# Optimization experiments

Hardware: AMD Instinct MI355X
Metric: run time of the kernel (lower is better)

Reference implementation:

```python
import jax, jax.numpy as jnp
import numpy as np

N_NODES = 50000
N_EDGES = 800000
D_IN = 128
D_HID = 128
N_CLASSES = 40


def setup_inputs() -> dict:
    key = jax.random.key(0)
    ks = jax.random.split(key, 12)
    x = jax.random.normal(ks[0], (N_NODES, D_IN), dtype=jnp.float32)
    edge_index = jax.random.randint(ks[1], (2, N_EDGES), 0, N_NODES, dtype=jnp.int64)
    s1 = 1.0 / np.sqrt(D_IN)
    s2 = 1.0 / np.sqrt(D_HID)
    W1 = jax.random.uniform(ks[2], (D_IN, D_HID), jnp.float32, -s1, s1)
    b1 = jnp.zeros((D_HID,), jnp.float32)
    W2 = jax.random.uniform(ks[3], (D_HID, D_HID), jnp.float32, -s2, s2)
    b2 = jnp.zeros((D_HID,), jnp.float32)
    W3 = jax.random.uniform(ks[4], (D_HID, D_HID), jnp.float32, -s2, s2)
    b3 = jnp.zeros((D_HID,), jnp.float32)
    fcW = jax.random.uniform(ks[5], (D_HID, N_CLASSES), jnp.float32, -s2, s2)
    fcb = jax.random.uniform(ks[6], (N_CLASSES,), jnp.float32, -s2, s2)
    return {"x": x, "edge_index": edge_index, "W1": W1, "b1": b1,
            "W2": W2, "b2": b2, "W3": W3, "b3": b3, "fcW": fcW, "fcb": fcb}


def _gcn_norm(edge_index, n_nodes):
    # add self-loops, compute symmetric normalization deg^-1/2[src]*deg^-1/2[dst]
    loops = jnp.arange(n_nodes, dtype=edge_index.dtype)
    src = jnp.concatenate([edge_index[0], loops])
    dst = jnp.concatenate([edge_index[1], loops])
    deg = jax.ops.segment_sum(jnp.ones_like(dst, dtype=jnp.float32), dst,
                              num_segments=n_nodes)
    dinv = jax.lax.rsqrt(deg)  # deg >= 1 thanks to self-loops
    norm = dinv[src] * dinv[dst]  # [E+N]
    return src, dst, norm


def _gcn_conv(h, W, b, src, dst, norm, n_nodes):
    h = h @ W                               # [N, D]
    msg = h[src] * norm[:, None]            # [E+N, D] gather + scale
    out = jax.ops.segment_sum(msg, dst, num_segments=n_nodes)  # scatter-add
    return out + b


def reference(x, edge_index, W1, b1, W2, b2, W3, b3, fcW, fcb):
    n = x.shape[0]
    src, dst, norm = _gcn_norm(edge_index, n)
    h = jax.nn.relu(_gcn_conv(x, W1, b1, src, dst, norm, n))
    h = jax.nn.relu(_gcn_conv(h, W2, b2, src, dst, norm, n))
    h = jax.nn.relu(_gcn_conv(h, W3, b3, src, dst, norm, n))
    out = h @ fcW + fcb
    return (h, out)
```

## Files before the change

### kernel.cpp

```cpp
#include <hip/hip_runtime.h>
#include <hip/hip_fp16.h>

#define NN 50000
#define NE 800000
#define D  128
#define NC 40
#define NBLK ((NN + 255) / 256)
#define NXCD 8
#define DRANGE ((NN + NXCD - 1) / NXCD)
#define EPB 2048
#define NCH ((NE + EPB - 1) / EPB)
#define CAP 64

typedef short bf16x8 __attribute__((ext_vector_type(8)));
typedef float f32x16 __attribute__((ext_vector_type(16)));

__device__ __forceinline__ void load_edge(const void* ei, int e, int is64, int& s, int& d) {
    if (is64) {
        const long long* p = (const long long*)ei;
        s = (int)p[e]; d = (int)p[NE + e];
    } else {
        const int* p = (const int*)ei;
        s = p[e]; d = p[NE + e];
    }
}

__global__ __launch_bounds__(256) void init_cnt_kernel(int* __restrict__ cnt) {
    int i = blockIdx.x * 256 + threadIdx.x;
    if (i < NN) cnt[i] = 0;
}

__global__ void detect_kernel(const int* ei, int* flag) {
    __shared__ int nz;
    if (threadIdx.x == 0) nz = 0;
    __syncthreads();
    int c = 0;
    for (int i = threadIdx.x; i < 2048; i += 256)
        if (ei[2 * i + 1] != 0) c = 1;
    if (c) atomicAdd(&nz, 1);
    __syncthreads();
    if (threadIdx.x == 0) *flag = (nz == 0) ? 1 : 0;
}

__global__ __launch_bounds__(256) void fill_kernel(const void* ei, const int* __restrict__ flag,
                                                   int* cnt, int* __restrict__ srcs) {
    int r = blockIdx.x & (NXCD - 1);
    int chunk = blockIdx.x >> 3;
    int base = chunk * EPB;
    int dlo = r * DRANGE, dhi = dlo + DRANGE;
    int is64 = *flag;
#pragma unroll
    for (int j = 0; j < EPB / 256; ++j) {
        int e = base + threadIdx.x + j * 256;
        if (e >= NE) break;
        int s, d; load_edge(ei, e, is64, s, d);
        if (d < dlo || d >= dhi || (unsigned)d >= NN || (unsigned)s >= NN) continue;
        int slot = atomicAdd(&cnt[d], 1);
        if (slot < CAP) srcs[d * CAP + slot] = s;
    }
}

__global__ __launch_bounds__(256) void sort_kernel(const int* __restrict__ cnt,
                                                   int* __restrict__ srcs) {
    int wid = (blockIdx.x * 256 + threadIdx.x) >> 6;
    int lane = threadIdx.x & 63;
    if (wid >= NN) return;
    int deg = cnt[wid]; if (deg > CAP) deg = CAP;
    if (deg <= 1) return;
    int base = wid * CAP;
    int v = (lane < deg) ? srcs[base + lane] : 0x7fffffff;
#pragma unroll
    for (int k = 2; k <= 64; k <<= 1) {
#pragma unroll
        for (int j = k >> 1; j > 0; j >>= 1) {
            int o = __shfl_xor(v, j);
            bool up = ((lane & k) == 0);
            bool lower = ((lane & j) == 0);
            int mn = min(v, o), mx = max(v, o);
            v = (lower == up) ? mn : mx;
        }
    }
    if (lane < deg) srcs[base + lane] = v;
}

__global__ __launch_bounds__(256) void dinv_kernel(const int* __restrict__ cnt,
                                                   float* __restrict__ dinv) {
    int i = blockIdx.x * 256 + threadIdx.x;
    if (i < NN) dinv[i] = 1.0f / sqrtf((float)cnt[i] + 1.0f);
}

__device__ __forceinline__ ushort f2bf(float x) {
    unsigned u = __float_as_uint(x);
    return (ushort)((u + 0x7fffu + ((u >> 16) & 1u)) >> 16);
}
__device__ __forceinline__ float bf2f(ushort h) {
    return __uint_as_float(((unsigned)h) << 16);
}

__global__ __launch_bounds__(128) void prep_w_kernel(const float* __restrict__ W,
                                                     ushort* __restrict__ img) {
    int c = blockIdx.x;
    int k = threadIdx.x;
    float w = W[(size_t)k * D + c];
    ushort hi = f2bf(w);
    ushort lo = f2bf(w - bf2f(hi));
    int ch = k >> 6, kk = k & 63, g = kk >> 3;
    int idx = c * 64 + ((g ^ (c & 7)) * 8) + (kk & 7);
    img[(size_t)(ch * 2 + 0) * 8192 + idx] = hi;
    img[(size_t)(ch * 2 + 1) * 8192 + idx] = lo;
}

__global__ __launch_bounds__(128) void prep_fcw_kernel(const float* __restrict__ W,
                                                       ushort* __restrict__ img) {
    int c = blockIdx.x;
    int k = threadIdx.x;
    float w = (c < NC) ? W[(size_t)k * NC + c] : 0.0f;
    ushort hi = f2bf(w);
    ushort lo = f2bf(w - bf2f(hi));
    int g = k >> 3;
    int idx = c * 128 + ((g ^ (c & 7)) * 8) + (k & 7);
    img[idx] = hi;
    img[8192 + idx] = lo;
}

__global__ __launch_bounds__(256, 2) void gemm_mfma_kernel(const float* __restrict__ A,
                                                           const ushort* __restrict__ Wimg,
                                                           ushort* __restrict__ T) {
    __shared__ alignas(16) ushort sAh[8192];
    __shared__ alignas(16) ushort sAl[8192];
    __shared__ alignas(16) ushort sWh[8192];
    __shared__ alignas(16) ushort sWl[8192];
    int tid = threadIdx.x;
    int wave = tid >> 6, lane = tid & 63;
    int wr = wave >> 1, wc = wave & 1;
    int m0 = blockIdx.x * 128;
    f32x16 acc[2][2];
#pragma unroll
    for (int i = 0; i < 2; ++i)
#pragma unroll
        for (int j = 0; j < 2; ++j)
#pragma unroll
            for (int q = 0; q < 16; ++q) acc[i][j][q] = 0.0f;

    for (int ch = 0; ch < 2; ++ch) {
        const float4* wh = (const float4*)(Wimg + (size_t)(ch * 2 + 0) * 8192);
        const float4* wl = (const float4*)(Wimg + (size_t)(ch * 2 + 1) * 8192);
#pragma unroll
        for (int i = 0; i < 4; ++i) {
            ((float4*)sWh)[tid + i * 256] = wh[tid + i * 256];
            ((float4*)sWl)[tid + i * 256] = wl[tid + i * 256];
        }
#pragma unroll
        for (int p = 0; p < 8; ++p) {
            int idx = tid + p * 256;
            int r = idx >> 4;
            int kq = idx & 15;
            float4 v = make_float4(0, 0, 0, 0);
            int grow = m0 + r;
            if (grow < NN) v = *(const float4*)(A + (size_t)grow * D + ch * 64 + kq * 4);
            ushort4 h, l;
            h.x = f2bf(v.x); l.x = f2bf(v.x - bf2f(h.x));
            h.y = f2bf(v.y); l.y = f2bf(v.y - bf2f(h.y));
            h.z = f2bf(v.z); l.z = f2bf(v.z - bf2f(h.z));
            h.w = f2bf(v.w); l.w = f2bf(v.w - bf2f(h.w));
            int g = kq >> 1, half = kq & 1;
            int uidx = r * 64 + ((g ^ (r & 7)) * 8) + half * 4;
            *(ushort4*)&sAh[uidx] = h;
            *(ushort4*)&sAl[uidx] = l;
        }
        __syncthreads();

        int rb = wr * 64 + (lane & 31);
        int cb = wc * 64 + (lane & 31);
#pragma unroll
        for (int s = 0; s < 4; ++s) {
            int gg = s * 2 + (lane >> 5);
            int ra0 = rb, ra1 = rb + 32;
            int ca0 = cb, ca1 = cb + 32;
            bf16x8 ah0 = *(const bf16x8*)&sAh[ra0 * 64 + ((gg ^ (ra0 & 7)) * 8)];
            bf16x8 ah1 = *(const bf16x8*)&sAh[ra1 * 64 + ((gg ^ (ra1 & 7)) * 8)];
            bf16x8 al0 = *(const bf16x8*)&sAl[ra0 * 64 + ((gg ^ (ra0 & 7)) * 8)];
            bf16x8 al1 = *(const bf16x8*)&sAl[ra1 * 64 + ((gg ^ (ra1 & 7)) * 8)];
            bf16x8 wh0 = *(const bf16x8*)&sWh[ca0 * 64 + ((gg ^ (ca0 & 7)) * 8)];
            bf16x8 wh1 = *(const bf16x8*)&sWh[ca1 * 64 + ((gg ^ (ca1 & 7)) * 8)];
            bf16x8 wl0 = *(const bf16x8*)&sWl[ca0 * 64 + ((gg ^ (ca0 & 7)) * 8)];
            bf16x8 wl1 = *(const bf16x8*)&sWl[ca1 * 64 + ((gg ^ (ca1 & 7)) * 8)];
            acc[0][0] = __builtin_amdgcn_mfma_f32_32x32x16_bf16(ah0, wh0, acc[0][0], 0, 0, 0);
            acc[0][0] = __builtin_amdgcn_mfma_f32_32x32x16_bf16(ah0, wl0, acc[0][0], 0, 0, 0);
            acc[0][0] = __builtin_amdgcn_mfma_f32_32x32x16_bf16(al0, wh0, acc[0][0], 0, 0, 0);
            acc[0][1] = __builtin_amdgcn_mfma_f32_32x32x16_bf16(ah0, wh1, acc[0][1], 0, 0, 0);
            acc[0][1] = __builtin_amdgcn_mfma_f32_32x32x16_bf16(ah0, wl1, acc[0][1], 0, 0, 0);
            acc[0][1] = __builtin_amdgcn_mfma_f32_32x32x16_bf16(al0, wh1, acc[0][1], 0, 0, 0);
            acc[1][0] = __builtin_amdgcn_mfma_f32_32x32x16_bf16(ah1, wh0, acc[1][0], 0, 0, 0);
            acc[1][0] = __builtin_amdgcn_mfma_f32_32x32x16_bf16(ah1, wl0, acc[1][0], 0, 0, 0);
            acc[1][0] = __builtin_amdgcn_mfma_f32_32x32x16_bf16(al1, wh0, acc[1][0], 0, 0, 0);
            acc[1][1] = __builtin_amdgcn_mfma_f32_32x32x16_bf16(ah1, wh1, acc[1][1], 0, 0, 0);
            acc[1][1] = __builtin_amdgcn_mfma_f32_32x32x16_bf16(ah1, wl1, acc[1][1], 0, 0, 0);
            acc[1][1] = __builtin_amdgcn_mfma_f32_32x32x16_bf16(al1, wh1, acc[1][1], 0, 0, 0);
        }
        __syncthreads();
    }
#pragma unroll
    for (int rt = 0; rt < 2; ++rt)
#pragma unroll
        for (int ct = 0; ct < 2; ++ct) {
            int cg = wc * 64 + ct * 32 + (lane & 31);
#pragma unroll
            for (int reg = 0; reg < 16; ++reg) {
                int row = m0 + wr * 64 + rt * 32 + (reg & 3) + 8 * (reg >> 2) + 4 * (lane >> 5);
                if (row < NN)
                    T[(size_t)row * D + cg] = __half_as_ushort(__float2half(acc[rt][ct][reg]));
            }
        }
}

__global__ __launch_bounds__(256, 2) void fc_mfma_kernel(const float* __restrict__ A,
                                                         const ushort* __restrict__ img,
                                                         const float* __restrict__ b,
                                                         float* __restrict__ O) {
    __shared__ alignas(16) ushort sAh[8192];
    __shared__ alignas(16) ushort sAl[8192];
    __shared__ alignas(16) ushort sWh[8192];
    __shared__ alignas(16) ushort sWl[8192];
    int tid = threadIdx.x;
    int wave = tid >> 6, lane = tid & 63;
    int m0 = blockIdx.x * 128;
#pragma unroll
    for (int i = 0; i < 4; ++i) {
        ((float4*)sWh)[tid + i * 256] = ((const float4*)img)[tid + i * 256];
        ((float4*)sWl)[tid + i * 256] = ((const float4*)(img + 8192))[tid + i * 256];
    }
    f32x16 acc[2];
#pragma unroll
    for (int j = 0; j < 2; ++j)
#pragma unroll
        for (int q = 0; q < 16; ++q) acc[j][q] = 0.0f;

    for (int ch = 0; ch < 2; ++ch) {
#pragma unroll
        for (int p = 0; p < 8; ++p) {
            int idx = tid + p * 256;
            int r = idx >> 4;
            int kq = idx & 15;
            float4 v = make_float4(0, 0, 0, 0);
            int grow = m0 + r;
            if (grow < NN) v = *(const float4*)(A + (size_t)grow * D + ch * 64 + kq * 4);
            ushort4 h, l;
            h.x = f2bf(v.x); l.x = f2bf(v.x - bf2f(h.x));
            h.y = f2bf(v.y); l.y = f2bf(v.y - bf2f(h.y));
            h.z = f2bf(v.z); l.z = f2bf(v.z - bf2f(h.z));
            h.w = f2bf(v.w); l.w = f2bf(v.w - bf2f(h.w));
            int g = kq >> 1, half = kq & 1;
            int uidx = r * 64 + ((g ^ (r & 7)) * 8) + half * 4;
            *(ushort4*)&sAh[uidx] = h;
            *(ushort4*)&sAl[uidx] = l;
        }
        __syncthreads();
        int ra = wave * 32 + (lane & 31);
        int c0 = lane & 31, c1 = 32 + (lane & 31);
#pragma unroll
        for (int s = 0; s < 4; ++s) {
            int gg = s * 2 + (lane >> 5);
            int kg = ch * 8 + gg;
            bf16x8 ah = *(const bf16x8*)&sAh[ra * 64 + ((gg ^ (ra & 7)) * 8)];
            bf16x8 al = *(const bf16x8*)&sAl[ra * 64 + ((gg ^ (ra & 7)) * 8)];
            bf16x8 wh0 = *(const bf16x8*)&sWh[c0 * 128 + ((kg ^ (c0 & 7)) * 8)];
            bf16x8 wl0 = *(const bf16x8*)&sWl[c0 * 128 + ((kg ^ (c0 & 7)) * 8)];
            bf16x8 wh1 = *(const bf16x8*)&sWh[c1 * 128 + ((kg ^ (c1 & 7)) * 8)];
            bf16x8 wl1 = *(const bf16x8*)&sWl[c1 * 128 + ((kg ^ (c1 & 7)) * 8)];
            acc[0] = __builtin_amdgcn_mfma_f32_32x32x16_bf16(ah, wh0, acc[0], 0, 0, 0);
            acc[0] = __builtin_amdgcn_mfma_f32_32x32x16_bf16(ah, wl0, acc[0], 0, 0, 0);
            acc[0] = __builtin_amdgcn_mfma_f32_32x32x16_bf16(al, wh0, acc[0], 0, 0, 0);
            acc[1] = __builtin_amdgcn_mfma_f32_32x32x16_bf16(ah, wh1, acc[1], 0, 0, 0);
            acc[1] = __builtin_amdgcn_mfma_f32_32x32x16_bf16(ah, wl1, acc[1], 0, 0, 0);
            acc[1] = __builtin_amdgcn_mfma_f32_32x32x16_bf16(al, wh1, acc[1], 0, 0, 0);
        }
        __syncthreads();
    }
#pragma unroll
    for (int ct = 0; ct < 2; ++ct) {
        int col = ct * 32 + (lane & 31);
        if (col < NC) {
            float bb = b[col];
#pragma unroll
            for (int reg = 0; reg < 16; ++reg) {
                int row = m0 + wave * 32 + (reg & 3) + 8 * (reg >> 2) + 4 * (lane >> 5);
                if (row < NN) O[(size_t)row * NC + col] = acc[ct][reg] + bb;
            }
        }
    }
}

__device__ __forceinline__ float4 h4load(const ushort* __restrict__ T, int row, int l) {
    uint2 hv = ((const uint2*)(T + (size_t)row * D))[l];
    __half2 h0 = *(__half2*)&hv.x, h1 = *(__half2*)&hv.y;
    float2 f0 = __half22float2(h0), f1 = __half22float2(h1);
    return make_float4(f0.x, f0.y, f1.x, f1.y);
}

__global__ __launch_bounds__(256) void aggregate_kernel(const ushort* __restrict__ T,
                                                        const int* __restrict__ cnt,
                                                        const int* __restrict__ srcs,
                                                        const float* __restrict__ dinv,
                                                        const float* __restrict__ b,
                                                        float* __restrict__ out) {
    int wid = (blockIdx.x * 256 + threadIdx.x) >> 6;
    int lane = threadIdx.x & 63;
    int h = lane >> 5, l = lane & 31;
    if (wid >= NN) return;
    float di = dinv[wid];
    float wself = h ? 0.0f : di * di;
    float4 acc = h4load(T, wid, l);
    acc.x *= wself; acc.y *= wself; acc.z *= wself; acc.w *= wself;
    int beg = wid * CAP;
    int deg = cnt[wid]; if (deg > CAP) deg = CAP;
    int end = beg + deg;
    int e = beg;
    for (; e + 7 < end; e += 8) {
        int s0 = srcs[e + h], s1 = srcs[e + 2 + h];
        int s2 = srcs[e + 4 + h], s3 = srcs[e + 6 + h];
        float w0 = dinv[s0] * di, w1 = dinv[s1] * di;
        float w2 = dinv[s2] * di, w3 = dinv[s3] * di;
        float4 v0 = h4load(T, s0, l);
        float4 v1 = h4load(T, s1, l);
        float4 v2 = h4load(T, s2, l);
        float4 v3 = h4load(T, s3, l);
        acc.x = fmaf(v0.x, w0, acc.x); acc.y = fmaf(v0.y, w0, acc.y);
        acc.z = fmaf(v0.z, w0, acc.z); acc.w = fmaf(v0.w, w0, acc.w);
        acc.x = fmaf(v1.x, w1, acc.x); acc.y = fmaf(v1.y, w1, acc.y);
        acc.z = fmaf(v1.z, w1, acc.z); acc.w = fmaf(v1.w, w1, acc.w);
        acc.x = fmaf(v2.x, w2, acc.x); acc.y = fmaf(v2.y, w2, acc.y);
        acc.z = fmaf(v2.z, w2, acc.z); acc.w = fmaf(v2.w, w2, acc.w);
        acc.x = fmaf(v3.x, w3, acc.x); acc.y = fmaf(v3.y, w3, acc.y);
        acc.z = fmaf(v3.z, w3, acc.z); acc.w = fmaf(v3.w, w3, acc.w);
    }
    for (; e + 1 < end; e += 2) {
        int s0 = srcs[e + h];
        float w0 = dinv[s0] * di;
        float4 v0 = h4load(T, s0, l);
        acc.x = fmaf(v0.x, w0, acc.x); acc.y = fmaf(v0.y, w0, acc.y);
        acc.z = fmaf(v0.z, w0, acc.z); acc.w = fmaf(v0.w, w0, acc.w);
    }
    if (e < end) {
        int ee = (e + h < end) ? e + h : end - 1;
        int s0 = srcs[ee];
        float w0 = (e + h < end) ? dinv[s0] * di : 0.0f;
        float4 v0 = h4load(T, s0, l);
        acc.x = fmaf(v0.x, w0, acc.x); acc.y = fmaf(v0.y, w0, acc.y);
        acc.z = fmaf(v0.z, w0, acc.z); acc.w = fmaf(v0.w, w0, acc.w);
    }
    acc.x += __shfl_xor(acc.x, 32);
    acc.y += __shfl_xor(acc.y, 32);
    acc.z += __shfl_xor(acc.z, 32);
    acc.w += __shfl_xor(acc.w, 32);
    if (h == 0) {
        float4 bb = ((const float4*)b)[l];
        acc.x = fmaxf(acc.x + bb.x, 0.0f);
        acc.y = fmaxf(acc.y + bb.y, 0.0f);
        acc.z = fmaxf(acc.z + bb.z, 0.0f);
        acc.w = fmaxf(acc.w + bb.w, 0.0f);
        ((float4*)(out + (size_t)wid * D))[l] = acc;
    }
}

extern "C" void kernel_launch(void* const* d_in, const int* in_sizes, int n_in,
                              void* d_out, int out_size, void* d_ws, size_t ws_size,
                              hipStream_t stream) {
    const float* x   = (const float*)d_in[0];
    const void*  ei  = d_in[1];
    const float* W1  = (const float*)d_in[2];
    const float* b1  = (const float*)d_in[3];
    const float* W2  = (const float*)d_in[4];
    const float* b2  = (const float*)d_in[5];
    const float* W3  = (const float*)d_in[6];
    const float* b3  = (const float*)d_in[7];
    const float* fcW = (const float*)d_in[8];
    const float* fcb = (const float*)d_in[9];

    float* out_h  = (float*)d_out;
    float* out_fc = out_h + (size_t)NN * D;

    size_t off = 0;
    auto alloc = [&](size_t bytes) {
        void* p = (char*)d_ws + off;
        off += (bytes + 255) & ~(size_t)255;
        return p;
    };
    float*  dinv   = (float*) alloc((size_t)NN * 4);
    int*    cnt    = (int*)   alloc((size_t)NN * 4);
    int*    flag   = (int*)   alloc(256);
    int*    srcs   = (int*)   alloc((size_t)NN * CAP * 4);
    ushort* bufT   = (ushort*)alloc((size_t)NN * D * 2);
    float*  bufH   = (float*) alloc((size_t)NN * D * 4);
    ushort* wimg1  = (ushort*)alloc(32768 * 2);
    ushort* wimg2  = (ushort*)alloc(32768 * 2);
    ushort* wimg3  = (ushort*)alloc(32768 * 2);
    ushort* fcimg  = (ushort*)alloc(16384 * 2);
    (void)ws_size; (void)in_sizes; (void)n_in; (void)out_size;

    init_cnt_kernel<<<NBLK, 256, 0, stream>>>(cnt);
    detect_kernel<<<1, 256, 0, stream>>>((const int*)ei, flag);
    prep_w_kernel<<<128, 128, 0, stream>>>(W1, wimg1);
    prep_w_kernel<<<128, 128, 0, stream>>>(W2, wimg2);
    prep_w_kernel<<<128, 128, 0, stream>>>(W3, wimg3);
    prep_fcw_kernel<<<64, 128, 0, stream>>>(fcW, fcimg);
    fill_kernel<<<NCH * NXCD, 256, 0, stream>>>(ei, flag, cnt, srcs);
    sort_kernel<<<(NN * 64 + 255) / 256, 256, 0, stream>>>(cnt, srcs);
    dinv_kernel<<<NBLK, 256, 0, stream>>>(cnt, dinv);

    auto layer = [&](const float* in, const ushort* wimg, const float* b, float* out) {
        gemm_mfma_kernel<<<(NN + 127) / 128, 256, 0, stream>>>(in, wimg, bufT);
        aggregate_kernel<<<(NN * 64 + 255) / 256, 256, 0, stream>>>(bufT, cnt, srcs, dinv, b, out);
    };

    layer(x,    wimg1, b1, bufH);
    layer(bufH, wimg2, b2, bufH);
    layer(bufH, wimg3, b3, out_h);

    fc_mfma_kernel<<<(NN + 127) / 128, 256, 0, stream>>>(out_h, fcimg, fcb, out_fc);
}
```

Before: 248.5 us.

## Emit pre-split bf16 tile images from aggregation and merge setup kernels

The hidden-layer aggregation now writes its output directly as a swizzled, tiled bf16 hi/lo split image, so the next GEMM can load its A tile straight into shared memory without a float-to-bf16 split pass. The float intermediate buffer is removed. Setup work is also consolidated: count init and int64 detection share one launch, the four weight-prep launches become one, and the dinv computation is folded into the sort kernel. Together these cut launch overhead and per-GEMM conversion work, at the cost of more template and layout complexity.

```diff
diff --git a/kernel.cpp b/kernel.cpp
--- a/kernel.cpp
+++ b/kernel.cpp
@@ -11,6 +11,7 @@
 #define EPB 2048
 #define NCH ((NE + EPB - 1) / EPB)
 #define CAP 64
+#define NTILE ((NN + 127) / 128)
 
 typedef short bf16x8 __attribute__((ext_vector_type(8)));
 typedef float f32x16 __attribute__((ext_vector_type(16)));
@@ -25,21 +26,23 @@
     }
 }
 
-__global__ __launch_bounds__(256) void init_cnt_kernel(int* __restrict__ cnt) {
-    int i = blockIdx.x * 256 + threadIdx.x;
-    if (i < NN) cnt[i] = 0;
-}
-
-__global__ void detect_kernel(const int* ei, int* flag) {
-    __shared__ int nz;
-    if (threadIdx.x == 0) nz = 0;
-    __syncthreads();
-    int c = 0;
-    for (int i = threadIdx.x; i < 2048; i += 256)
-        if (ei[2 * i + 1] != 0) c = 1;
-    if (c) atomicAdd(&nz, 1);
-    __syncthreads();
-    if (threadIdx.x == 0) *flag = (nz == 0) ? 1 : 0;
+__global__ __launch_bounds__(256) void setup_kernel(int* __restrict__ cnt,
+                                                    const int* __restrict__ ei,
+                                                    int* __restrict__ flag) {
+    if (blockIdx.x == NBLK) {
+        __shared__ int nz;
+        if (threadIdx.x == 0) nz = 0;
+        __syncthreads();
+        int c = 0;
+        for (int i = threadIdx.x; i < 2048; i += 256)
+            if (ei[2 * i + 1] != 0) c = 1;
+        if (c) atomicAdd(&nz, 1);
+        __syncthreads();
+        if (threadIdx.x == 0) *flag = (nz == 0) ? 1 : 0;
+    } else {
+        int i = blockIdx.x * 256 + threadIdx.x;
+        if (i < NN) cnt[i] = 0;
+    }
 }
 
 __global__ __launch_bounds__(256) void fill_kernel(const void* ei, const int* __restrict__ flag,
@@ -61,11 +64,14 @@
 }
 
 __global__ __launch_bounds__(256) void sort_kernel(const int* __restrict__ cnt,
-                                                   int* __restrict__ srcs) {
+                                                   int* __restrict__ srcs,
+                                                   float* __restrict__ dinv) {
     int wid = (blockIdx.x * 256 + threadIdx.x) >> 6;
     int lane = threadIdx.x & 63;
     if (wid >= NN) return;
-    int deg = cnt[wid]; if (deg > CAP) deg = CAP;
+    int deg_raw = cnt[wid];
+    if (lane == 0) dinv[wid] = 1.0f / sqrtf((float)deg_raw + 1.0f);
+    int deg = (deg_raw > CAP) ? CAP : deg_raw;
     if (deg <= 1) return;
     int base = wid * CAP;
     int v = (lane < deg) ? srcs[base + lane] : 0x7fffffff;
@@ -83,12 +89,6 @@
     if (lane < deg) srcs[base + lane] = v;
 }
 
-__global__ __launch_bounds__(256) void dinv_kernel(const int* __restrict__ cnt,
-                                                   float* __restrict__ dinv) {
-    int i = blockIdx.x * 256 + threadIdx.x;
-    if (i < NN) dinv[i] = 1.0f / sqrtf((float)cnt[i] + 1.0f);
-}
-
 __device__ __forceinline__ ushort f2bf(float x) {
     unsigned u = __float_as_uint(x);
     return (ushort)((u + 0x7fffu + ((u >> 16) & 1u)) >> 16);
@@ -97,35 +97,43 @@
     return __uint_as_float(((unsigned)h) << 16);
 }
 
-__global__ __launch_bounds__(128) void prep_w_kernel(const float* __restrict__ W,
-                                                     ushort* __restrict__ img) {
-    int c = blockIdx.x;
+__global__ __launch_bounds__(128) void prep_all_kernel(const float* __restrict__ W1,
+                                                       const float* __restrict__ W2,
+                                                       const float* __restrict__ W3,
+                                                       const float* __restrict__ fcW,
+                                                       ushort* __restrict__ i1,
+                                                       ushort* __restrict__ i2,
+                                                       ushort* __restrict__ i3,
+                                                       ushort* __restrict__ ifc) {
+    int b = blockIdx.x;
     int k = threadIdx.x;
-    float w = W[(size_t)k * D + c];
-    ushort hi = f2bf(w);
-    ushort lo = f2bf(w - bf2f(hi));
-    int ch = k >> 6, kk = k & 63, g = kk >> 3;
-    int idx = c * 64 + ((g ^ (c & 7)) * 8) + (kk & 7);
-    img[(size_t)(ch * 2 + 0) * 8192 + idx] = hi;
-    img[(size_t)(ch * 2 + 1) * 8192 + idx] = lo;
-}
-
-__global__ __launch_bounds__(128) void prep_fcw_kernel(const float* __restrict__ W,
-                                                       ushort* __restrict__ img) {
-    int c = blockIdx.x;
-    int k = threadIdx.x;
-    float w = (c < NC) ? W[(size_t)k * NC + c] : 0.0f;
-    ushort hi = f2bf(w);
-    ushort lo = f2bf(w - bf2f(hi));
-    int g = k >> 3;
-    int idx = c * 128 + ((g ^ (c & 7)) * 8) + (k & 7);
-    img[idx] = hi;
-    img[8192 + idx] = lo;
-}
-
-__global__ __launch_bounds__(256, 2) void gemm_mfma_kernel(const float* __restrict__ A,
-                                                           const ushort* __restrict__ Wimg,
-                                                           ushort* __restrict__ T) {
+    if (b < 384) {
+        const float* W = (b < 128) ? W1 : (b < 256) ? W2 : W3;
+        ushort* img = (b < 128) ? i1 : (b < 256) ? i2 : i3;
+        int c = b & 127;
+        float w = W[(size_t)k * D + c];
+        ushort hi = f2bf(w);
+        ushort lo = f2bf(w - bf2f(hi));
+        int ch = k >> 6, kk = k & 63, g = kk >> 3;
+        int idx = c * 64 + ((g ^ (c & 7)) * 8) + (kk & 7);
+        img[(size_t)(ch * 2 + 0) * 8192 + idx] = hi;
+        img[(size_t)(ch * 2 + 1) * 8192 + idx] = lo;
+    } else {
+        int c = b - 384;
+        float w = (c < NC) ? fcW[(size_t)k * NC + c] : 0.0f;
+        ushort hi = f2bf(w);
+        ushort lo = f2bf(w - bf2f(hi));
+        int g = k >> 3;
+        int idx = c * 128 + ((g ^ (c & 7)) * 8) + (k & 7);
+        ifc[idx] = hi;
+        ifc[8192 + idx] = lo;
+    }
+}
+
+
+__global__ __launch_bounds__(256, 2) void gemm_f32_kernel(const float* __restrict__ A,
+                                                          const ushort* __restrict__ Wimg,
+                                                          ushort* __restrict__ T) {
     __shared__ alignas(16) ushort sAh[8192];
     __shared__ alignas(16) ushort sAl[8192];
     __shared__ alignas(16) ushort sWh[8192];
@@ -214,6 +222,84 @@
         }
 }
 
+__global__ __launch_bounds__(256, 2) void gemm_img_kernel(const ushort* __restrict__ Aimg,
+                                                          const ushort* __restrict__ Wimg,
+                                                          ushort* __restrict__ T) {
+    __shared__ alignas(16) ushort sAh[8192];
+    __shared__ alignas(16) ushort sAl[8192];
+    __shared__ alignas(16) ushort sWh[8192];
+    __shared__ alignas(16) ushort sWl[8192];
+    int tid = threadIdx.x;
+    int wave = tid >> 6, lane = tid & 63;
+    int wr = wave >> 1, wc = wave & 1;
+    int m0 = blockIdx.x * 128;
+    const ushort* Atile = Aimg + (size_t)blockIdx.x * 32768;
+    f32x16 acc[2][2];
+#pragma unroll
+    for (int i = 0; i < 2; ++i)
+#pragma unroll
+        for (int j = 0; j < 2; ++j)
+#pragma unroll
+            for (int q = 0; q < 16; ++q) acc[i][j][q] = 0.0f;
+
+    for (int ch = 0; ch < 2; ++ch) {
+        const float4* wh = (const float4*)(Wimg + (size_t)(ch * 2 + 0) * 8192);
+        const float4* wl = (const float4*)(Wimg + (size_t)(ch * 2 + 1) * 8192);
+        const float4* ah = (const float4*)(Atile + (size_t)(ch * 2 + 0) * 8192);
+        const float4* al = (const float4*)(Atile + (size_t)(ch * 2 + 1) * 8192);
+#pragma unroll
+        for (int i = 0; i < 4; ++i) {
+            ((float4*)sWh)[tid + i * 256] = wh[tid + i * 256];
+            ((float4*)sWl)[tid + i * 256] = wl[tid + i * 256];
+            ((float4*)sAh)[tid + i * 256] = ah[tid + i * 256];
+            ((float4*)sAl)[tid + i * 256] = al[tid + i * 256];
+        }
+        __syncthreads();
+
+        int rb = wr * 64 + (lane & 31);
+        int cb = wc * 64 + (lane & 31);
+#pragma unroll
+        for (int s = 0; s < 4; ++s) {
+            int gg = s * 2 + (lane >> 5);
+            int ra0 = rb, ra1 = rb + 32;
+            int ca0 = cb, ca1 = cb + 32;
+            bf16x8 ah0 = *(const bf16x8*)&sAh[ra0 * 64 + ((gg ^ (ra0 & 7)) * 8)];
+            bf16x8 ah1 = *(const bf16x8*)&sAh[ra1 * 64 + ((gg ^ (ra1 & 7)) * 8)];
+            bf16x8 al0 = *(const bf16x8*)&sAl[ra0 * 64 + ((gg ^ (ra0 & 7)) * 8)];
+            bf16x8 al1 = *(const bf16x8*)&sAl[ra1 * 64 + ((gg ^ (ra1 & 7)) * 8)];
+            bf16x8 wh0 = *(const bf16x8*)&sWh[ca0 * 64 + ((gg ^ (ca0 & 7)) * 8)];
+            bf16x8 wh1 = *(const bf16x8*)&sWh[ca1 * 64 + ((gg ^ (ca1 & 7)) * 8)];
+            bf16x8 wl0 = *(const bf16x8*)&sWl[ca0 * 64 + ((gg ^ (ca0 & 7)) * 8)];
+            bf16x8 wl1 = *(const bf16x8*)&sWl[ca1 * 64 + ((gg ^ (ca1 & 7)) * 8)];
+            acc[0][0] = __builtin_amdgcn_mfma_f32_32x32x16_bf16(ah0, wh0, acc[0][0], 0, 0, 0);
+            acc[0][0] = __builtin_amdgcn_mfma_f32_32x32x16_bf16(ah0, wl0, acc[0][0], 0, 0, 0);
+            acc[0][0] = __builtin_amdgcn_mfma_f32_32x32x16_bf16(al0, wh0, acc[0][0], 0, 0, 0);
+            acc[0][1] = __builtin_amdgcn_mfma_f32_32x32x16_bf16(ah0, wh1, acc[0][1], 0, 0, 0);
+            acc[0][1] = __builtin_amdgcn_mfma_f32_32x32x16_bf16(ah0, wl1, acc[0][1], 0, 0, 0);
+            acc[0][1] = __builtin_amdgcn_mfma_f32_32x32x16_bf16(al0, wh1, acc[0][1], 0, 0, 0);
+            acc[1][0] = __builtin_amdgcn_mfma_f32_32x32x16_bf16(ah1, wh0, acc[1][0], 0, 0, 0);
+            acc[1][0] = __builtin_amdgcn_mfma_f32_32x32x16_bf16(ah1, wl0, acc[1][0], 0, 0, 0);
+            acc[1][0] = __builtin_amdgcn_mfma_f32_32x32x16_bf16(al1, wh0, acc[1][0], 0, 0, 0);
+            acc[1][1] = __builtin_amdgcn_mfma_f32_32x32x16_bf16(ah1, wh1, acc[1][1], 0, 0, 0);
+            acc[1][1] = __builtin_amdgcn_mfma_f32_32x32x16_bf16(ah1, wl1, acc[1][1], 0, 0, 0);
+            acc[1][1] = __builtin_amdgcn_mfma_f32_32x32x16_bf16(al1, wh1, acc[1][1], 0, 0, 0);
+        }
+        __syncthreads();
+    }
+#pragma unroll
+    for (int rt = 0; rt < 2; ++rt)
+#pragma unroll
+        for (int ct = 0; ct < 2; ++ct) {
+            int cg = wc * 64 + ct * 32 + (lane & 31);
+#pragma unroll
+            for (int reg = 0; reg < 16; ++reg) {
+                int row = m0 + wr * 64 + rt * 32 + (reg & 3) + 8 * (reg >> 2) + 4 * (lane >> 5);
+                if (row < NN)
+                    T[(size_t)row * D + cg] = __half_as_ushort(__float2half(acc[rt][ct][reg]));
+            }
+        }
+}
+
 __global__ __launch_bounds__(256, 2) void fc_mfma_kernel(const float* __restrict__ A,
                                                          const ushort* __restrict__ img,
                                                          const float* __restrict__ b,
@@ -298,12 +384,14 @@
     return make_float4(f0.x, f0.y, f1.x, f1.y);
 }
 
+template<int IMG>
 __global__ __launch_bounds__(256) void aggregate_kernel(const ushort* __restrict__ T,
                                                         const int* __restrict__ cnt,
                                                         const int* __restrict__ srcs,
                                                         const float* __restrict__ dinv,
                                                         const float* __restrict__ b,
-                                                        float* __restrict__ out) {
+                                                        float* __restrict__ out,
+                                                        ushort* __restrict__ img) {
     int wid = (blockIdx.x * 256 + threadIdx.x) >> 6;
     int lane = threadIdx.x & 63;
     int h = lane >> 5, l = lane & 31;
@@ -359,7 +447,22 @@
         acc.y = fmaxf(acc.y + bb.y, 0.0f);
         acc.z = fmaxf(acc.z + bb.z, 0.0f);
         acc.w = fmaxf(acc.w + bb.w, 0.0f);
-        ((float4*)(out + (size_t)wid * D))[l] = acc;
+        if (IMG) {
+            int tile = wid >> 7, rr = wid & 127;
+            int c0 = 4 * l;
+            int ch = c0 >> 6, kk = c0 & 63, g = kk >> 3;
+            int idx = rr * 64 + ((g ^ (rr & 7)) * 8) + (kk & 7);
+            ushort4 hh, ll;
+            hh.x = f2bf(acc.x); ll.x = f2bf(acc.x - bf2f(hh.x));
+            hh.y = f2bf(acc.y); ll.y = f2bf(acc.y - bf2f(hh.y));
+            hh.z = f2bf(acc.z); ll.z = f2bf(acc.z - bf2f(hh.z));
+            hh.w = f2bf(acc.w); ll.w = f2bf(acc.w - bf2f(hh.w));
+            ushort* base = img + (size_t)tile * 32768;
+            *(ushort4*)(base + (size_t)(ch * 2 + 0) * 8192 + idx) = hh;
+            *(ushort4*)(base + (size_t)(ch * 2 + 1) * 8192 + idx) = ll;
+        } else {
+            ((float4*)(out + (size_t)wid * D))[l] = acc;
+        }
     }
 }
 
@@ -391,31 +494,25 @@
     int*    flag   = (int*)   alloc(256);
     int*    srcs   = (int*)   alloc((size_t)NN * CAP * 4);
     ushort* bufT   = (ushort*)alloc((size_t)NN * D * 2);
-    float*  bufH   = (float*) alloc((size_t)NN * D * 4);
+    ushort* himg   = (ushort*)alloc((size_t)NTILE * 32768 * 2);
     ushort* wimg1  = (ushort*)alloc(32768 * 2);
     ushort* wimg2  = (ushort*)alloc(32768 * 2);
     ushort* wimg3  = (ushort*)alloc(32768 * 2);
     ushort* fcimg  = (ushort*)alloc(16384 * 2);
     (void)ws_size; (void)in_sizes; (void)n_in; (void)out_size;
 
-    init_cnt_kernel<<<NBLK, 256, 0, stream>>>(cnt);
-    detect_kernel<<<1, 256, 0, stream>>>((const int*)ei, flag);
-    prep_w_kernel<<<128, 128, 0, stream>>>(W1, wimg1);
-    prep_w_kernel<<<128, 128, 0, stream>>>(W2, wimg2);
-    prep_w_kernel<<<128, 128, 0, stream>>>(W3, wimg3);
-    prep_fcw_kernel<<<64, 128, 0, stream>>>(fcW, fcimg);
+    setup_kernel<<<NBLK + 1, 256, 0, stream>>>(cnt, (const int*)ei, flag);
+    prep_all_kernel<<<448, 128, 0, stream>>>(W1, W2, W3, fcW, wimg1, wimg2, wimg3, fcimg);
     fill_kernel<<<NCH * NXCD, 256, 0, stream>>>(ei, flag, cnt, srcs);
-    sort_kernel<<<(NN * 64 + 255) / 256, 256, 0, stream>>>(cnt, srcs);
-    dinv_kernel<<<NBLK, 256, 0, stream>>>(cnt, dinv);
-
-    auto layer = [&](const float* in, const ushort* wimg, const float* b, float* out) {
-        gemm_mfma_kernel<<<(NN + 127) / 128, 256, 0, stream>>>(in, wimg, bufT);
-        aggregate_kernel<<<(NN * 64 + 255) / 256, 256, 0, stream>>>(bufT, cnt, srcs, dinv, b, out);
-    };
-
-    layer(x,    wimg1, b1, bufH);
-    layer(bufH, wimg2, b2, bufH);
-    layer(bufH, wimg3, b3, out_h);
-
-    fc_mfma_kernel<<<(NN + 127) / 128, 256, 0, stream>>>(out_h, fcimg, fcb, out_fc);
-}
+    sort_kernel<<<(NN * 64 + 255) / 256, 256, 0, stream>>>(cnt, srcs, dinv);
+
+    int agg_grid = (NN * 64 + 255) / 256;
+    gemm_f32_kernel<<<NTILE, 256, 0, stream>>>(x, wimg1, bufT);
+    aggregate_kernel<1><<<agg_grid, 256, 0, stream>>>(bufT, cnt, srcs, dinv, b1, nullptr, himg);
+    gemm_img_kernel<<<NTILE, 256, 0, stream>>>(himg, wimg2, bufT);
+    aggregate_kernel<1><<<agg_grid, 256, 0, stream>>>(bufT, cnt, srcs, dinv, b2, nullptr, himg);
+    gemm_img_kernel<<<NTILE, 256, 0, stream>>>(himg, wimg3, bufT);
+    aggregate_kernel<0><<<agg_grid, 256, 0, stream>>>(bufT, cnt, srcs, dinv, b3, out_h, nullptr);
+
+    fc_mfma_kernel<<<NTILE, 256, 0, stream>>>(out_h, fcimg, fcb, out_fc);
+}
```

After: 232.1 us. 6.6% less time.
